# Performance work log

Hardware: AMD Instinct MI355X
Metric: run time of the kernel (lower is better)

## Reference

```python
import jax, jax.numpy as jnp
import numpy as np

T, B, IN_DIM = 2048, 8, 512
D_VALUE, D_KEY = 512, 128
CHUNK = 128
EPS = 1e-8


def setup_inputs() -> dict:
    key = jax.random.key(0)
    ks = jax.random.split(key, 9)
    s = 0.02
    return {
        "x": jax.random.normal(ks[0], (T, B, IN_DIM), dtype=jnp.float32),
        "Wv": jax.random.normal(ks[1], (D_VALUE, IN_DIM), dtype=jnp.float32) * s,
        "bv": jnp.zeros((D_VALUE,), dtype=jnp.float32),
        "Wk": jax.random.normal(ks[2], (D_KEY, IN_DIM), dtype=jnp.float32) * s,
        "bk": jnp.zeros((D_KEY,), dtype=jnp.float32),
        "Wq": jax.random.normal(ks[3], (D_KEY, IN_DIM), dtype=jnp.float32) * s,
        "bq": jnp.zeros((D_KEY,), dtype=jnp.float32),
        "Wa": jax.random.normal(ks[4], (D_KEY, IN_DIM), dtype=jnp.float32) * s,
        "ba": jnp.zeros((D_KEY,), dtype=jnp.float32),
    }


def _gla_forward(x, Wv, bv, Wk, bk, Wq, bq, Wa, ba):
    # Projections: x (T,B,in) -> v (T,B,d), k/q/alpha (T,B,n)
    v = jnp.einsum("tbi,di->tbd", x, Wv) + bv
    k = jnp.einsum("tbi,ni->tbn", x, Wk) + bk
    q = jnp.einsum("tbi,ni->tbn", x, Wq) + bq
    alpha = jax.nn.sigmoid(jnp.einsum("tbi,ni->tbn", x, Wa) + ba)

    Tt, Bb, d = v.shape
    n = k.shape[2]
    nch = Tt // CHUNK  # T chosen divisible by CHUNK

    # Reshape time-major tensors into (n_chunks, C, B, dim)
    v_r = v.reshape(nch, CHUNK, Bb, d)
    k_r = k.reshape(nch, CHUNK, Bb, n)
    q_r = q.reshape(nch, CHUNK, Bb, n)
    a_r = alpha.reshape(nch, CHUNK, Bb, n)

    def chunk_step(S_prev, inp):
        v_ch, k_ch, q_ch, a_ch = inp  # (C,B,d), (C,B,n), (C,B,n), (C,B,n)
        outer = jnp.einsum("tbd,tbn->tbdn", v_ch, k_ch)  # (C,B,d,n)
        cp = jnp.cumprod(jnp.maximum(a_ch, EPS), axis=0)  # (C,B,n)
        inv_prefix = 1.0 / (cp + EPS)
        scaled = jnp.cumsum(outer * inv_prefix[:, :, None, :], axis=0)
        # local decayed state plus carried state decayed by prefix product
        S_local = (scaled + S_prev[None, :, :, :]) * cp[:, :, None, :]
        y_ch = jnp.einsum("tbdn,tbn->tbd", S_local, q_ch)  # S @ q
        return S_local[-1], y_ch

    S0 = jnp.zeros((Bb, d, n), dtype=v.dtype)
    _, y = jax.lax.scan(chunk_step, S0, (v_r, k_r, q_r, a_r))
    return y.reshape(Tt, Bb, d)


def reference(x, Wv, bv, Wk, bk, Wq, bq, Wa, ba):
    return _gla_forward(x, Wv, bv, Wk, bk, Wq, bq, Wa, ba)
```

## Files before the change

### kernel.cpp

```cpp
#include <hip/hip_runtime.h>


#define EPSV 1e-8f

typedef __bf16 bf16x8 __attribute__((ext_vector_type(8)));
typedef __bf16 bf16x4 __attribute__((ext_vector_type(4)));
typedef float f32x4 __attribute__((ext_vector_type(4)));

__device__ __forceinline__ void async_copy16(const void* g, void* l) {
  __builtin_amdgcn_global_load_lds(
      (const __attribute__((address_space(1))) void*)g,
      (__attribute__((address_space(3))) void*)l, 16, 0, 0);
}

__global__ __launch_bounds__(256) void conv_all(const float* __restrict__ x,
                                                const float* __restrict__ Wv,
                                                const float* __restrict__ Wk,
                                                const float* __restrict__ Wq,
                                                const float* __restrict__ Wa,
                                                __bf16* __restrict__ xb,
                                                __bf16* __restrict__ wcat) {
  if (blockIdx.x < 4096) {
    long i = ((long)blockIdx.x * 256 + threadIdx.x) * 8;
    float4 f0 = *(const float4*)(x + i);
    float4 f1 = *(const float4*)(x + i + 4);
    bf16x8 h;
    h[0] = (__bf16)f0.x; h[1] = (__bf16)f0.y; h[2] = (__bf16)f0.z; h[3] = (__bf16)f0.w;
    h[4] = (__bf16)f1.x; h[5] = (__bf16)f1.y; h[6] = (__bf16)f1.z; h[7] = (__bf16)f1.w;
    *(bf16x8*)(xb + i) = h;
  } else {
    long i = ((long)(blockIdx.x - 4096) * 256 + threadIdx.x) * 8;
    int row = (int)(i >> 9);
    int col = (int)(i & 511);
    const float* src;
    if (row < 512)      src = Wv + (long)row * 512 + col;
    else if (row < 640) src = Wk + (long)(row - 512) * 512 + col;
    else if (row < 768) src = Wq + (long)(row - 640) * 512 + col;
    else                src = Wa + (long)(row - 768) * 512 + col;
    float4 f0 = *(const float4*)(src);
    float4 f1 = *(const float4*)(src + 4);
    bf16x8 h;
    h[0] = (__bf16)f0.x; h[1] = (__bf16)f0.y; h[2] = (__bf16)f0.z; h[3] = (__bf16)f0.w;
    h[4] = (__bf16)f1.x; h[5] = (__bf16)f1.y; h[6] = (__bf16)f1.z; h[7] = (__bf16)f1.w;
    *(bf16x8*)(wcat + i) = h;
  }
}

__global__ __launch_bounds__(256) void proj_mfma(
    const __bf16* __restrict__ xb, const __bf16* __restrict__ wcat,
    const float* __restrict__ bv, const float* __restrict__ bk,
    const float* __restrict__ bq, const float* __restrict__ ba,
    __bf16* __restrict__ vt, __bf16* __restrict__ kout,
    __bf16* __restrict__ qout, float* __restrict__ aout) {
  __shared__ __attribute__((aligned(16))) char smem[128 * 136 * 2];
  __bf16* a_sm = (__bf16*)smem;
  __bf16* b_sm = a_sm + 128 * 64;
  __bf16* tr   = (__bf16*)smem;

  int tid = threadIdx.x;
  int lane = tid & 63, wave = tid >> 6;
  int bid = blockIdx.x;
  int xr = bid & 7, sq = bid >> 3;
  int mt = xr + 8 * (sq / 7);
  int nt = sq % 7;
  int wr = wave >> 1, wcol = wave & 1;

  const __bf16* xtile = xb + (long)mt * 128 * 512;
  const __bf16* wtile = wcat + (long)nt * 128 * 512;

  f32x4 acc[4][4] = {};
  int lr8 = lane >> 3, lc8 = lane & 7;
  int l15 = lane & 15, qd = lane >> 4;
  int slsrc = (lc8 ^ lr8) * 8;
  int frd = l15 & 7;

  for (int k0 = 0; k0 < 512; k0 += 64) {
#pragma unroll
    for (int h = 0; h < 4; ++h) {
      int q = wave * 4 + h;
      int row = q * 8 + lr8;
      async_copy16(xtile + (long)row * 512 + k0 + slsrc, &a_sm[q * 512]);
      async_copy16(wtile + (long)row * 512 + k0 + slsrc, &b_sm[q * 512]);
    }
    __syncthreads();
#pragma unroll
    for (int kk = 0; kk < 2; ++kk) {
      bf16x8 af[4], bfr[4];
#pragma unroll
      for (int t = 0; t < 4; ++t) {
        int ra = wr * 64 + t * 16 + l15;
        int rb = wcol * 64 + t * 16 + l15;
        int slot = ((kk * 4 + qd) ^ frd) * 8;
        af[t]  = *(const bf16x8*)&a_sm[ra * 64 + slot];
        bfr[t] = *(const bf16x8*)&b_sm[rb * 64 + slot];
      }
#pragma unroll
      for (int i = 0; i < 4; ++i)
#pragma unroll
        for (int j = 0; j < 4; ++j)
          acc[i][j] = __builtin_amdgcn_mfma_f32_16x16x32_bf16(af[i], bfr[j], acc[i][j], 0, 0, 0);
    }
    __syncthreads();
  }

  if (nt < 4) {
    const float* bias = bv + nt * 128;
#pragma unroll
    for (int i = 0; i < 4; ++i)
#pragma unroll
      for (int j = 0; j < 4; ++j) {
        int col = wcol * 64 + j * 16 + l15;
        float bz = bias[col];
#pragma unroll
        for (int r = 0; r < 4; ++r) {
          int row = wr * 64 + i * 16 + qd * 4 + r;
          tr[col * 136 + (row & 7) * 16 + (row >> 3)] = (__bf16)(acc[i][j][r] + bz);
        }
      }
    __syncthreads();
    int cbase = (mt >> 3) * 8;
    int s0 = (mt & 7) * 16;
#pragma unroll
    for (int it = 0; it < 4; ++it) {
      int p = it * 256 + tid;
      int d = p & 127, b = p >> 7;
      bf16x8 u0 = *(const bf16x8*)&tr[d * 136 + b * 16];
      bf16x8 u1 = *(const bf16x8*)&tr[d * 136 + b * 16 + 8];
      __bf16* dst = vt + ((long)(cbase + b) * 512 + nt * 128 + d) * 128 + s0;
      *(bf16x8*)dst = u0;
      *(bf16x8*)(dst + 8) = u1;
    }
    return;
  }

  const float* bias; bool sig = false;
  __bf16* dstb = nullptr; float* dstf = nullptr;
  if (nt == 4)      { bias = bk; dstb = kout; }
  else if (nt == 5) { bias = bq; dstb = qout; }
  else              { bias = ba; dstf = aout; sig = true; }

#pragma unroll
  for (int i = 0; i < 4; ++i)
#pragma unroll
    for (int j = 0; j < 4; ++j) {
      int col = wcol * 64 + j * 16 + l15;
      float bz = bias[col];
#pragma unroll
      for (int r = 0; r < 4; ++r) {
        int row = wr * 64 + i * 16 + qd * 4 + r;
        float z = acc[i][j][r] + bz;
        long addr = ((long)mt * 128 + row) * 128 + col;
        if (sig) dstf[addr] = 1.f / (1.f + __expf(-z));
        else     dstb[addr] = (__bf16)z;
      }
    }
}

__global__ __launch_bounds__(512) void scan_cp(const float* __restrict__ a,
                                               const __bf16* __restrict__ k,
                                               const __bf16* __restrict__ q,
                                               __bf16* __restrict__ kbs,
                                               __bf16* __restrict__ qb,
                                               __bf16* __restrict__ kt,
                                               float* __restrict__ cpend) {
  __shared__ float segprod[8][64];
  int tid = threadIdx.x;
  int nl = tid & 63;
  int seg = tid >> 6;
  int bid = blockIdx.x;
  int nh = bid & 1;
  int b = (bid >> 1) & 7;
  int c = bid >> 4;
  int n = nh * 64 + nl;
  long base = ((long)c * 1024 + b) * 128 + n;
  int t0 = seg * 16;

  float av[16];
  float p = 1.f;
#pragma unroll
  for (int i = 0; i < 16; ++i) {
    float v = fmaxf(a[base + (long)(t0 + i) * 1024], EPSV);
    av[i] = v;
    p *= v;
  }
  segprod[seg][nl] = p;
  __syncthreads();

  float prefix = 1.f;
#pragma unroll
  for (int s = 0; s < 7; ++s)
    if (s < seg) prefix *= segprod[s][nl];
  if (seg == 7) cpend[(c * 8 + b) * 128 + n] = prefix * p;

  float cp = prefix;
  __bf16 ktbuf[16];
#pragma unroll
  for (int i = 0; i < 16; ++i) {
    long off = base + (long)(t0 + i) * 1024;
    cp *= av[i];
    float kk = (float)k[off] / (cp + EPSV);
    float qq = (float)q[off] * cp;
    __bf16 kh = (__bf16)kk;
    kbs[off] = kh;
    qb[off] = (__bf16)qq;
    ktbuf[i] = kh;
  }
  __bf16* dst = kt + ((long)((c * 8 + b) * 128 + n)) * 128 + t0;
#pragma unroll
  for (int i = 0; i < 2; ++i) {
    bf16x8 h;
#pragma unroll
    for (int j = 0; j < 8; ++j) h[j] = ktbuf[i * 8 + j];
    *(bf16x8*)(dst + i * 8) = h;
  }
}

__global__ __launch_bounds__(256) void gmm(const __bf16* __restrict__ vt,
                                           const __bf16* __restrict__ kt,
                                           const float* __restrict__ cpend,
                                           __bf16* __restrict__ Gt) {
  __shared__ __attribute__((aligned(16))) __bf16 v_sm[128 * 128];
  __shared__ __attribute__((aligned(16))) __bf16 k_sm[128 * 128];
  int tid = threadIdx.x, lane = tid & 63, wave = tid >> 6;
  int wr = wave >> 1, wc = wave & 1;
  int l15 = lane & 15, qd = lane >> 4;
  int cb = blockIdx.x >> 2, dt = blockIdx.x & 3;
  const __bf16* vbase = vt + ((long)cb * 512 + dt * 128) * 128;
  const __bf16* kbase = kt + (long)cb * 16384;

  int rowoff = lane >> 4, sl = lane & 15;
#pragma unroll
  for (int it = 0; it < 8; ++it) {
    int rbase = it * 16 + wave * 4;
    int row = rbase + rowoff;
    int sg = (sl ^ (row & 15)) * 8;
    async_copy16(vbase + (long)row * 128 + sg, &v_sm[rbase * 128]);
    async_copy16(kbase + (long)row * 128 + sg, &k_sm[rbase * 128]);
  }
  __syncthreads();

  f32x4 acc[4][4] = {};
#pragma unroll
  for (int kk = 0; kk < 4; ++kk) {
    bf16x8 af[4], bfr[4];
#pragma unroll
    for (int i = 0; i < 4; ++i) {
      int ra = wr * 64 + i * 16 + l15;
      af[i] = *(const bf16x8*)&v_sm[ra * 128 + (((kk * 4 + qd) ^ l15) & 15) * 8];
    }
#pragma unroll
    for (int j = 0; j < 4; ++j) {
      int rb = wc * 64 + j * 16 + l15;
      bfr[j] = *(const bf16x8*)&k_sm[rb * 128 + (((kk * 4 + qd) ^ l15) & 15) * 8];
    }
#pragma unroll
    for (int i = 0; i < 4; ++i)
#pragma unroll
      for (int j = 0; j < 4; ++j)
        acc[i][j] = __builtin_amdgcn_mfma_f32_16x16x32_bf16(af[i], bfr[j], acc[i][j], 0, 0, 0);
  }
  float ce[4];
#pragma unroll
  for (int j = 0; j < 4; ++j) ce[j] = cpend[cb * 128 + wc * 64 + j * 16 + l15];
#pragma unroll
  for (int i = 0; i < 4; ++i)
#pragma unroll
    for (int j = 0; j < 4; ++j) {
      int col = wc * 64 + j * 16 + l15;
#pragma unroll
      for (int r = 0; r < 4; ++r) {
        int row = wr * 64 + i * 16 + qd * 4 + r;
        Gt[((long)cb * 512 + dt * 128 + row) * 128 + col] = (__bf16)(acc[i][j][r] * ce[j]);
      }
    }
}

__global__ __launch_bounds__(256) void scan_state(const __bf16* __restrict__ Gt,
                                                  const float* __restrict__ cpend,
                                                  __bf16* __restrict__ St) {
  long e = ((long)blockIdx.x * 256 + threadIdx.x) * 4;
  int n0 = (int)(e & 127);
  int b = (int)(e >> 16);
  float4 S = {0.f, 0.f, 0.f, 0.f};
#pragma unroll
  for (int c = 0; c < 16; ++c) {
    long idx = (long)c * 524288 + e;
    bf16x4 g = *(const bf16x4*)(Gt + idx);
    bf16x4 sv;
    sv[0] = (__bf16)S.x; sv[1] = (__bf16)S.y;
    sv[2] = (__bf16)S.z; sv[3] = (__bf16)S.w;
    *(bf16x4*)(St + idx) = sv;
    const float4 cp = *(const float4*)(cpend + (c * 8 + b) * 128 + n0);
    S.x = (float)g[0] + S.x * cp.x;
    S.y = (float)g[1] + S.y * cp.y;
    S.z = (float)g[2] + S.z * cp.z;
    S.w = (float)g[3] + S.w * cp.w;
  }
}

__global__ __launch_bounds__(256) void ymm(const __bf16* __restrict__ qb,
                                           const __bf16* __restrict__ kbs,
                                           const __bf16* __restrict__ vt,
                                           const __bf16* __restrict__ St,
                                           float* __restrict__ out) {
  __shared__ __attribute__((aligned(16))) __bf16 q_sm[128 * 128];
  __shared__ __attribute__((aligned(16))) __bf16 A_lds[128 * 136];
  int tid = threadIdx.x, lane = tid & 63, wave = tid >> 6;
  int wr = wave >> 1, wc = wave & 1;
  int l15 = lane & 15, qd = lane >> 4;
  int cb = blockIdx.x >> 2, dt = blockIdx.x & 3;
  int c = cb >> 3, b = cb & 7;
  const __bf16* qg = qb + ((long)c * 1024 + b) * 128;
  const __bf16* kg = kbs + ((long)c * 1024 + b) * 128;
  const __bf16* vbase = vt + ((long)cb * 512 + dt * 128) * 128;
  const __bf16* sbase = St + ((long)cb * 512 + dt * 128) * 128;
  int rowoff = lane >> 4, sl = lane & 15;

#pragma unroll
  for (int it = 0; it < 8; ++it) {
    int rbase = it * 16 + wave * 4;
    int row = rbase + rowoff;
    int sg = (sl ^ (row & 15)) * 8;
    async_copy16(qg + (long)row * 1024 + sg, &q_sm[rbase * 128]);
  }
  __syncthreads();

  {
    f32x4 accA[4][4] = {};
#pragma unroll
    for (int kk = 0; kk < 4; ++kk) {
      int k0 = kk * 32;
      bf16x8 af[4], bfr[4];
#pragma unroll
      for (int i = 0; i < 4; ++i) {
        int ra = wr * 64 + i * 16 + l15;
        af[i] = *(const bf16x8*)&q_sm[ra * 128 + (((kk * 4 + qd) ^ l15) & 15) * 8];
      }
#pragma unroll
      for (int j = 0; j < 4; ++j) {
        int rb = wc * 64 + j * 16 + l15;
        bfr[j] = *(const bf16x8*)(kg + (long)rb * 1024 + k0 + qd * 8);
      }
#pragma unroll
      for (int i = 0; i < 4; ++i)
#pragma unroll
        for (int j = 0; j < 4; ++j)
          accA[i][j] = __builtin_amdgcn_mfma_f32_16x16x32_bf16(af[i], bfr[j], accA[i][j], 0, 0, 0);
    }
#pragma unroll
    for (int i = 0; i < 4; ++i)
#pragma unroll
      for (int j = 0; j < 4; ++j) {
        int s = wc * 64 + j * 16 + l15;
#pragma unroll
        for (int r = 0; r < 4; ++r) {
          int t = wr * 64 + i * 16 + qd * 4 + r;
          A_lds[t * 136 + s] = (s <= t) ? (__bf16)accA[i][j][r] : (__bf16)0.f;
        }
      }
  }
  __syncthreads();

  f32x4 acc[4][4] = {};
#pragma unroll
  for (int kk = 0; kk < 4; ++kk) {
    int k0 = kk * 32;
    bf16x8 af[4], bfr[4];
#pragma unroll
    for (int i = 0; i < 4; ++i) {
      int ra = wr * 64 + i * 16 + l15;
      af[i] = *(const bf16x8*)(vbase + (long)ra * 128 + k0 + qd * 8);
    }
#pragma unroll
    for (int j = 0; j < 4; ++j)
      bfr[j] = *(const bf16x8*)&A_lds[(wc * 64 + j * 16 + l15) * 136 + k0 + qd * 8];
#pragma unroll
    for (int i = 0; i < 4; ++i)
#pragma unroll
      for (int j = 0; j < 4; ++j)
        acc[i][j] = __builtin_amdgcn_mfma_f32_16x16x32_bf16(af[i], bfr[j], acc[i][j], 0, 0, 0);
  }

#pragma unroll
  for (int kk = 0; kk < 4; ++kk) {
    int k0 = kk * 32;
    bf16x8 af[4], bfr[4];
#pragma unroll
    for (int i = 0; i < 4; ++i) {
      int ra = wr * 64 + i * 16 + l15;
      af[i] = *(const bf16x8*)(sbase + (long)ra * 128 + k0 + qd * 8);
    }
#pragma unroll
    for (int j = 0; j < 4; ++j) {
      int rb = wc * 64 + j * 16 + l15;
      bfr[j] = *(const bf16x8*)&q_sm[rb * 128 + (((kk * 4 + qd) ^ l15) & 15) * 8];
    }
#pragma unroll
    for (int i = 0; i < 4; ++i)
#pragma unroll
      for (int j = 0; j < 4; ++j)
        acc[i][j] = __builtin_amdgcn_mfma_f32_16x16x32_bf16(af[i], bfr[j], acc[i][j], 0, 0, 0);
  }

#pragma unroll
  for (int i = 0; i < 4; ++i)
#pragma unroll
    for (int j = 0; j < 4; ++j) {
      int colt = wc * 64 + j * 16 + l15;
      long addr = ((long)(c * 128 + colt) * 8 + b) * 512 + dt * 128 + wr * 64 + i * 16 + qd * 4;
      *(float4*)(out + addr) = *(float4*)&acc[i][j];
    }
}

extern "C" void kernel_launch(void* const* d_in, const int* in_sizes, int n_in,
                              void* d_out, int out_size, void* d_ws, size_t ws_size,
                              hipStream_t stream) {
  const float* x  = (const float*)d_in[0];
  const float* Wv = (const float*)d_in[1];
  const float* bv = (const float*)d_in[2];
  const float* Wk = (const float*)d_in[3];
  const float* bk = (const float*)d_in[4];
  const float* Wq = (const float*)d_in[5];
  const float* bq = (const float*)d_in[6];
  const float* Wa = (const float*)d_in[7];
  const float* ba = (const float*)d_in[8];
  float* out = (float*)d_out;
  float* ws = (float*)d_ws;

  float*  a_buf = ws;
  __bf16* qb    = (__bf16*)(ws + 2097152);
  __bf16* kbs   = (__bf16*)(ws + 3145728);
  __bf16* kt    = (__bf16*)(ws + 4194304);
  __bf16* vt    = (__bf16*)(ws + 5242880);
  __bf16* k_raw = (__bf16*)(ws + 9437184);
  __bf16* q_raw = (__bf16*)(ws + 10485760);
  __bf16* xb    = (__bf16*)(ws + 11534336);
  __bf16* Wcat  = (__bf16*)(ws + 15728640);
  __bf16* Gt    = xb;
  __bf16* St    = (__bf16*)(ws + 15958016);
  float*  cpend = ws + 20152320;

  conv_all<<<4320, 256, 0, stream>>>(x, Wv, Wk, Wq, Wa, xb, Wcat);
  proj_mfma<<<896, 256, 0, stream>>>(xb, Wcat, bv, bk, bq, ba,
                                     vt, k_raw, q_raw, a_buf);
  scan_cp<<<256, 512, 0, stream>>>(a_buf, k_raw, q_raw, kbs, qb, kt, cpend);
  gmm<<<512, 256, 0, stream>>>(vt, kt, cpend, Gt);
  scan_state<<<512, 256, 0, stream>>>(Gt, cpend, St);
  ymm<<<512, 256, 0, stream>>>(qb, kbs, vt, St, out);
}
```

Baseline: 173.6 us.

## Register-prefetch next K tile in projection GEMM instead of direct global-to-LDS copies

The projection GEMM main loop no longer issues async global_load_lds copies and then waits on them. It now loads the next 64-wide K slice into registers while the MFMAs for the current slice run, then stores those registers into swizzled LDS at the top of the next iteration. The goal is to hide global load latency behind compute, at the cost of more VGPRs and an extra register-to-LDS store step. It also changes the per-thread row mapping and the barrier placement.

Result: slower. 228.2 us (+31.4%).

```diff
diff --git a/kernel.cpp b/kernel.cpp
--- a/kernel.cpp
+++ b/kernel.cpp
@@ -69,20 +69,39 @@
   const __bf16* wtile = wcat + (long)nt * 128 * 512;
 
   f32x4 acc[4][4] = {};
-  int lr8 = lane >> 3, lc8 = lane & 7;
   int l15 = lane & 15, qd = lane >> 4;
-  int slsrc = (lc8 ^ lr8) * 8;
   int frd = l15 & 7;
 
-  for (int k0 = 0; k0 < 512; k0 += 64) {
+  int lrow = tid >> 3;
+  int c8 = tid & 7;
+  int swsl = (c8 ^ (lrow & 7)) * 8;
+
+  uint4 rA[4], rB[4];
+#pragma unroll
+  for (int h = 0; h < 4; ++h) {
+    int row = lrow + h * 32;
+    rA[h] = *(const uint4*)(xtile + (long)row * 512 + c8 * 8);
+    rB[h] = *(const uint4*)(wtile + (long)row * 512 + c8 * 8);
+  }
+
+  for (int it = 0; it < 8; ++it) {
+    __syncthreads();
 #pragma unroll
     for (int h = 0; h < 4; ++h) {
-      int q = wave * 4 + h;
-      int row = q * 8 + lr8;
-      async_copy16(xtile + (long)row * 512 + k0 + slsrc, &a_sm[q * 512]);
-      async_copy16(wtile + (long)row * 512 + k0 + slsrc, &b_sm[q * 512]);
+      int row = lrow + h * 32;
+      *(uint4*)&a_sm[row * 64 + swsl] = rA[h];
+      *(uint4*)&b_sm[row * 64 + swsl] = rB[h];
     }
     __syncthreads();
+    if (it < 7) {
+      int k0 = (it + 1) * 64;
+#pragma unroll
+      for (int h = 0; h < 4; ++h) {
+        int row = lrow + h * 32;
+        rA[h] = *(const uint4*)(xtile + (long)row * 512 + k0 + c8 * 8);
+        rB[h] = *(const uint4*)(wtile + (long)row * 512 + k0 + c8 * 8);
+      }
+    }
 #pragma unroll
     for (int kk = 0; kk < 2; ++kk) {
       bf16x8 af[4], bfr[4];
@@ -100,8 +119,8 @@
         for (int j = 0; j < 4; ++j)
           acc[i][j] = __builtin_amdgcn_mfma_f32_16x16x32_bf16(af[i], bfr[j], acc[i][j], 0, 0, 0);
     }
-    __syncthreads();
-  }
+  }
+  __syncthreads();
 
   if (nt < 4) {
     const float* bias = bv + nt * 128;
```
